# Kernel optimization log

Measured on AMD Instinct MI355X. Metric: run time of the kernel, lower is better.

Reference implementation:

```python
import jax, jax.numpy as jnp
import numpy as np

N = 32768; G = 64; PER = N // G; E = 262144; H = 128; HEADS = 4; DH = H // HEADS

def _leaky(x):
    return jnp.where(x > 0, x, 0.01 * x)

def _bn(x, w, b, eps=1e-5):
    mu = jnp.mean(x, 0)
    var = jnp.var(x, 0)  # biased, as torch BatchNorm1d uses for normalization
    return (x - mu) * jax.lax.rsqrt(var + eps) * w + b

def setup_inputs():
    key = jax.random.key(0)
    ks = jax.random.split(key, 20)
    s = 0.05
    g = jax.random.randint(ks[0], (E,), 0, G)
    src = g * PER + jax.random.randint(ks[1], (E,), 0, PER)
    dst = g * PER + jax.random.randint(ks[2], (E,), 0, PER)
    return {
        'node_fts': jax.random.normal(ks[3], (N, H)),
        'edge_attr': jax.random.normal(ks[4], (E, H)),
        'graph_fts': jax.random.normal(ks[5], (G, H)),
        'hidden': jax.random.normal(ks[6], (N, H)),
        'W_ee': jax.random.normal(ks[7], (H, H)) * s, 'b_ee': jnp.zeros((H,)),
        'M0': jax.random.normal(ks[8], (6 * H, H)) * s,
        'M1': jax.random.normal(ks[9], (H, H)) * s,
        'M2': jax.random.normal(ks[10], (H, H)) * s,
        'M3': jax.random.normal(ks[11], (H, H)) * s,
        'U1': jax.random.normal(ks[12], (2 * H, H)) * s,
        'U2': jax.random.normal(ks[13], (H, H)) * s,
        'Wqkv': jax.random.normal(ks[14], (H, 3 * H)) * s, 'bqkv': jnp.zeros((3 * H,)),
        'Wo': jax.random.normal(ks[15], (H, H)) * s, 'bo': jnp.zeros((H,)),
        'bn1_w': jnp.ones((H,)), 'bn1_b': jnp.zeros((H,)),
        'bn2_w': jnp.ones((H,)), 'bn2_b': jnp.zeros((H,)),
        'bn3_w': jnp.ones((H,)), 'bn3_b': jnp.zeros((H,)),
        'W1': jax.random.normal(ks[16], (H, 2 * H)) * s, 'b1': jnp.zeros((2 * H,)),
        'W2': jax.random.normal(ks[17], (2 * H, H)) * s, 'b2': jnp.zeros((H,)),
        'edge_index': jnp.stack([src, dst]),
        'batch': jnp.arange(N, dtype=jnp.int32) // PER,
    }

def _forward(node_fts, edge_attr, graph_fts, hidden, W_ee, b_ee, M0, M1, M2, M3,
             U1, U2, Wqkv, bqkv, Wo, bo, bn1_w, bn1_b, bn2_w, bn2_b,
             bn3_w, bn3_b, W1, b1, W2, b2, edge_index, batch):
    src, dst = edge_index[0], edge_index[1]
    ea = edge_attr @ W_ee + b_ee                            # GPS.edge_emb  [E,H]
    z = jnp.concatenate([node_fts, hidden], axis=-1)        # [N,2H]
    gfi = graph_fts[batch[dst]]                             # graph_fts_i   [E,H]
    # MPNN message: cat(x_i, x_j, edge_attr, graph_fts_i) -> 4-layer MLP, no bias
    m = jnp.concatenate([z[dst], z[src], ea, gfi], axis=-1) # [E,6H]
    m = m @ M0
    m = _leaky(m) @ M1
    m = _leaky(m) @ M2
    m = _leaky(m) @ M3                                      # [E,H]
    agg = jax.ops.segment_max(m, dst, num_segments=N)
    agg = jnp.where(jnp.isfinite(agg), agg, 0.0)            # PyG max-aggr: 0 for empty segments
    h_local = z @ U1 + agg @ U2                             # MPNN.update (use_gate=False)
    h1 = _bn(h_local + node_fts, bn1_w, bn1_b)              # GPSConv residual + norm1
    # global multihead attention over dense per-graph batches (all graphs exactly PER nodes)
    xd = node_fts.reshape(G, PER, H)
    q, k, v = jnp.split(xd @ Wqkv + bqkv, 3, axis=-1)
    q = q.reshape(G, PER, HEADS, DH).transpose(0, 2, 1, 3)
    k = k.reshape(G, PER, HEADS, DH).transpose(0, 2, 1, 3)
    v = v.reshape(G, PER, HEADS, DH).transpose(0, 2, 1, 3)
    att = jax.nn.softmax(jnp.einsum('ghqd,ghkd->ghqk', q, k) / float(np.sqrt(DH)), axis=-1)
    o = jnp.einsum('ghqk,ghkd->ghqd', att, v).transpose(0, 2, 1, 3).reshape(N, H)
    o = o @ Wo + bo
    h2 = _bn(o + node_fts, bn2_w, bn2_b)                    # residual + norm2
    out = h1 + h2
    out = out + (jax.nn.relu(out @ W1 + b1) @ W2 + b2)      # GPSConv MLP residual
    return _bn(out, bn3_w, bn3_b)                           # norm3

def reference(node_fts, edge_attr, graph_fts, hidden, W_ee, b_ee, M0, M1, M2, M3,
              U1, U2, Wqkv, bqkv, Wo, bo, bn1_w, bn1_b, bn2_w, bn2_b,
              bn3_w, bn3_b, W1, b1, W2, b2, edge_index, batch):
    return _forward(node_fts, edge_attr, graph_fts, hidden, W_ee, b_ee, M0, M1, M2, M3,
                    U1, U2, Wqkv, bqkv, Wo, bo, bn1_w, bn1_b, bn2_w, bn2_b,
                    bn3_w, bn3_b, W1, b1, W2, b2, edge_index, batch)
```

## Files before the change

### kernel.cpp

```cpp
#include <hip/hip_runtime.h>

typedef unsigned short u16;
typedef unsigned int u32;

#define NN 32768
#define EE 262144
#define HH 128
#define INV_N (1.0f / 32768.0f)
#define BN_EPS 1e-5f
#define ENC_NEGINF 0x007FFFFFu

typedef __attribute__((ext_vector_type(8))) __bf16 bf16x8;
typedef __attribute__((ext_vector_type(4))) float f32x4;

#define OFF_WEE 0
#define OFF_M0 16384
#define OFF_M1 114688
#define OFF_M2 131072
#define OFF_M3 147456
#define OFF_U 163840
#define OFF_QKV 212992
#define OFF_WO 262144
#define OFF_W1T 278528
#define OFF_W2T 311296
#define WT_ELEMS 344064

#define WS_AGG 0u
#define WS_OUTB 0u
#define WS_Y3 8388608u
#define WS_QKV 16777216u
#define WS_Y1 16777216u
#define WS_Y2 25165824u
#define WS_STATS 41943040u
#define WS_WT 41946112u

__device__ __forceinline__ float bf2f(u16 u) {
  union { u32 u; float f; } x; x.u = ((u32)u) << 16; return x.f;
}
__device__ __forceinline__ u16 f2bf(float f) {
  union { float f; u32 u; } x; x.f = f;
  return (u16)((x.u + 0x7FFFu + ((x.u >> 16) & 1u)) >> 16);
}
__device__ __forceinline__ u32 encf(float f) {
  union { float f; u32 u; } x; x.f = f;
  return (x.u & 0x80000000u) ? ~x.u : (x.u | 0x80000000u);
}
__device__ __forceinline__ float decf(u32 u) {
  union { u32 u; float f; } x;
  x.u = (u & 0x80000000u) ? (u ^ 0x80000000u) : ~u;
  return x.f;
}
__device__ __forceinline__ bf16x8 ld_frag(const u16* p) {
  return __builtin_bit_cast(bf16x8, *(const uint4*)p);
}
__device__ __forceinline__ uint4 pack8(const float* p) {
  u32 o0 = (u32)f2bf(p[0]) | ((u32)f2bf(p[1]) << 16);
  u32 o1 = (u32)f2bf(p[2]) | ((u32)f2bf(p[3]) << 16);
  u32 o2 = (u32)f2bf(p[4]) | ((u32)f2bf(p[5]) << 16);
  u32 o3 = (u32)f2bf(p[6]) | ((u32)f2bf(p[7]) << 16);
  return make_uint4(o0, o1, o2, o3);
}

template <int NCT>
__device__ __forceinline__ void mfma_step(const u16* As, int astride, int ka,
                                          const u16* Ws, int wstride, int kw,
                                          f32x4* acc, int lane, int wrow) {
  const int q = lane >> 4, cl = lane & 15;
  bf16x8 a = ld_frag(As + (wrow + cl) * astride + ka + q * 8);
#pragma unroll
  for (int ct = 0; ct < NCT; ++ct) {
    bf16x8 b = ld_frag(Ws + (ct * 16 + cl) * wstride + kw + q * 8);
    acc[ct] = __builtin_amdgcn_mfma_f32_16x16x32_bf16(a, b, acc[ct], 0, 0, 0);
  }
}

template <int NCT>
__device__ __forceinline__ void mfma_chunk128(const u16* A0, const u16* A1,
                                              const u16* Ws, int wstride,
                                              f32x4* acc, int lane, int wrow) {
  mfma_step<NCT>(A0, 72, 0, Ws, wstride, 0, acc, lane, wrow);
  mfma_step<NCT>(A0, 72, 32, Ws, wstride, 32, acc, lane, wrow);
  mfma_step<NCT>(A1, 72, 0, Ws, wstride, 64, acc, lane, wrow);
  mfma_step<NCT>(A1, 72, 32, Ws, wstride, 96, acc, lane, wrow);
}

__device__ __forceinline__ void stageA64f(u16* dst, const float* src, int rs, int tid) {
#pragma unroll
  for (int i = 0; i < 2; ++i) {
    int idx = tid + i * 256, r = idx >> 3, s = idx & 7;
    *(uint4*)(dst + r * 72 + s * 8) = pack8(src + (size_t)r * rs + s * 8);
  }
}
__device__ __forceinline__ void stageA64gf(u16* dst, const float* base,
                                           const int* rows, int co, int tid) {
#pragma unroll
  for (int i = 0; i < 2; ++i) {
    int idx = tid + i * 256, r = idx >> 3, s = idx & 7;
    *(uint4*)(dst + r * 72 + s * 8) = pack8(base + (size_t)rows[r] * HH + co + s * 8);
  }
}
__device__ __forceinline__ void stageA64(u16* dst, const u16* src, int rs, int tid) {
#pragma unroll
  for (int i = 0; i < 2; ++i) {
    int idx = tid + i * 256, r = idx >> 3, s = idx & 7;
    *(uint4*)(dst + r * 72 + s * 8) = *(const uint4*)(src + (size_t)r * rs + s * 8);
  }
}
__device__ __forceinline__ void stageA128(u16* dst, const u16* src, int tid) {
#pragma unroll
  for (int i = 0; i < 4; ++i) {
    int idx = tid + i * 256, r = idx >> 4, s = idx & 15;
    *(uint4*)(dst + r * 136 + s * 8) = *(const uint4*)(src + (size_t)r * HH + s * 8);
  }
}
template <int NR, int KW, int DS>
__device__ __forceinline__ void stageW(u16* dst, const u16* wt, int K, int koff, int tid) {
  constexpr int SEGS = KW / 8;
  constexpr int ITER = NR * SEGS / 256;
#pragma unroll
  for (int i = 0; i < ITER; ++i) {
    int idx = tid + i * 256;
    int c = idx / SEGS, s = idx % SEGS;
    *(uint4*)(dst + c * DS + s * 8) = *(const uint4*)(wt + (size_t)c * K + koff + s * 8);
  }
}
__device__ __forceinline__ void stage_agg(u16* dst, const u32* src, int tid) {
#pragma unroll
  for (int i = 0; i < 2; ++i) {
    int idx = tid + i * 256, r = idx >> 3, s = idx & 7;
    const u32* p = src + (size_t)r * HH + s * 8;
    u32 o[4];
#pragma unroll
    for (int j = 0; j < 4; ++j) {
      u32 u0 = p[2 * j], u1 = p[2 * j + 1];
      float f0 = (u0 == ENC_NEGINF) ? 0.f : decf(u0);
      float f1 = (u1 == ENC_NEGINF) ? 0.f : decf(u1);
      o[j] = (u32)f2bf(f0) | ((u32)f2bf(f1) << 16);
    }
    *(uint4*)(dst + r * 72 + s * 8) = make_uint4(o[0], o[1], o[2], o[3]);
  }
}


__global__ __launch_bounds__(256) void k_init(u32* __restrict__ agg,
                                              float* __restrict__ stats) {
  int gid = blockIdx.x * 256 + threadIdx.x;
  *(uint4*)(agg + (size_t)gid * 4) =
      make_uint4(ENC_NEGINF, ENC_NEGINF, ENC_NEGINF, ENC_NEGINF);
  if (gid < 768) stats[gid] = 0.f;
}

__global__ __launch_bounds__(256) void k_transpose(
    const float* w_ee, const float* m0, const float* m1, const float* m2,
    const float* m3, const float* u1, const float* u2, const float* wqkv,
    const float* wo, const float* w1, const float* w2, u16* __restrict__ wt) {
  const float* src; int K, C, ds, dk; size_t doff;
  switch (blockIdx.y) {
    case 0: src = w_ee; K = 128; C = 128; doff = OFF_WEE; ds = 128; dk = 0; break;
    case 1: src = m0; K = 768; C = 128; doff = OFF_M0; ds = 768; dk = 0; break;
    case 2: src = m1; K = 128; C = 128; doff = OFF_M1; ds = 128; dk = 0; break;
    case 3: src = m2; K = 128; C = 128; doff = OFF_M2; ds = 128; dk = 0; break;
    case 4: src = m3; K = 128; C = 128; doff = OFF_M3; ds = 128; dk = 0; break;
    case 5: src = u1; K = 256; C = 128; doff = OFF_U; ds = 384; dk = 0; break;
    case 6: src = u2; K = 128; C = 128; doff = OFF_U; ds = 384; dk = 256; break;
    case 7: src = wqkv; K = 128; C = 384; doff = OFF_QKV; ds = 128; dk = 0; break;
    case 8: src = wo; K = 128; C = 128; doff = OFF_WO; ds = 128; dk = 0; break;
    case 9: src = w1; K = 128; C = 256; doff = OFF_W1T; ds = 128; dk = 0; break;
    default: src = w2; K = 256; C = 128; doff = OFF_W2T; ds = 256; dk = 0; break;
  }
  int gid = blockIdx.x * 256 + threadIdx.x;
  if (gid < K * C) {
    int k = gid / C, c = gid - k * C;
    wt[doff + (size_t)c * ds + dk + k] = f2bf(src[gid]);
  }
}

__global__ __launch_bounds__(256) void k_edge(
    const float* __restrict__ node_fts, const float* __restrict__ hidden,
    const float* __restrict__ edge_attr, const float* __restrict__ graph_fts,
    const float* __restrict__ b_ee, const u16* __restrict__ wt,
    const int* __restrict__ ei, u32* __restrict__ agg) {
  __shared__ u16 sA0[64 * 72], sA1[64 * 72], sW[128 * 136];
  __shared__ int sSrc[64], sDst[64], sG[64];
  const int tid = threadIdx.x, lane = tid & 63, w = tid >> 6, wrow = w * 16;
  const int q = lane >> 4, cl = lane & 15;
  const int e0 = blockIdx.x * 64;
  if (tid < 64) {
    sSrc[tid] = ei[e0 + tid];
    int d = ei[EE + e0 + tid];
    sDst[tid] = d;
    sG[tid] = d >> 9;
  }
  stageA64f(sA0, edge_attr + (size_t)e0 * HH, HH, tid);
  stageA64f(sA1, edge_attr + (size_t)e0 * HH + 64, HH, tid);
  stageW<128, 128, 136>(sW, wt + OFF_WEE, 128, 0, tid);
  __syncthreads();
  const f32x4 fz = {0.f, 0.f, 0.f, 0.f};
  f32x4 acc[8];
#pragma unroll
  for (int i = 0; i < 8; ++i) acc[i] = fz;
  mfma_chunk128<8>(sA0, sA1, sW, 136, acc, lane, wrow);
#pragma unroll
  for (int ct = 0; ct < 8; ++ct) {
    float bias = b_ee[ct * 16 + cl];
#pragma unroll
    for (int r = 0; r < 4; ++r) {
      int row = wrow + q * 4 + r, col = ct * 16 + cl;
      u16* t = (col < 64) ? sA0 : sA1;
      t[row * 72 + (col & 63)] = f2bf(acc[ct][r] + bias);
    }
  }
  __syncthreads();
  stageW<128, 128, 136>(sW, wt + OFF_M0, 768, 512, tid);
  __syncthreads();
#pragma unroll
  for (int i = 0; i < 8; ++i) acc[i] = fz;
  mfma_chunk128<8>(sA0, sA1, sW, 136, acc, lane, wrow);
  const float* bs[5] = {node_fts, hidden, node_fts, hidden, graph_fts};
  const int* rw[5] = {sDst, sDst, sSrc, sSrc, sG};
  const int ko[5] = {0, 128, 256, 384, 640};
#pragma unroll
  for (int c = 0; c < 5; ++c) {
    __syncthreads();
    stageA64gf(sA0, bs[c], rw[c], 0, tid);
    stageA64gf(sA1, bs[c], rw[c], 64, tid);
    stageW<128, 128, 136>(sW, wt + OFF_M0, 768, ko[c], tid);
    __syncthreads();
    mfma_chunk128<8>(sA0, sA1, sW, 136, acc, lane, wrow);
  }
  const int lo[3] = {OFF_M1, OFF_M2, OFF_M3};
#pragma unroll
  for (int l = 0; l < 3; ++l) {
#pragma unroll
    for (int ct = 0; ct < 8; ++ct) {
#pragma unroll
      for (int r = 0; r < 4; ++r) {
        float v = acc[ct][r];
        v = v > 0.f ? v : 0.01f * v;
        int row = wrow + q * 4 + r, col = ct * 16 + cl;
        u16* t = (col < 64) ? sA0 : sA1;
        t[row * 72 + (col & 63)] = f2bf(v);
      }
    }
    __syncthreads();
    stageW<128, 128, 136>(sW, wt + lo[l], 128, 0, tid);
    __syncthreads();
#pragma unroll
    for (int i = 0; i < 8; ++i) acc[i] = fz;
    mfma_chunk128<8>(sA0, sA1, sW, 136, acc, lane, wrow);
  }
#pragma unroll
  for (int ct = 0; ct < 8; ++ct) {
#pragma unroll
    for (int r = 0; r < 4; ++r) {
      int e_l = wrow + q * 4 + r, f = ct * 16 + cl;
      atomicMax(&agg[(size_t)sDst[e_l] * HH + f], encf(acc[ct][r]));
    }
  }
}

__global__ __launch_bounds__(256) void k_y1(const float* __restrict__ node_fts,
                                            const float* __restrict__ hidden,
                                            const u32* __restrict__ agg,
                                            const u16* __restrict__ wt,
                                            u16* __restrict__ y1) {
  __shared__ u16 sA0[64 * 72], sA1[64 * 72], sW[128 * 136];
  const int tid = threadIdx.x, lane = tid & 63, w = tid >> 6, wrow = w * 16;
  const int q = lane >> 4, cl = lane & 15;
  const int nb = blockIdx.x * 64;
  const f32x4 fz = {0.f, 0.f, 0.f, 0.f};
  f32x4 acc[8];
#pragma unroll
  for (int i = 0; i < 8; ++i) acc[i] = fz;
  stageA64f(sA0, node_fts + (size_t)nb * HH, HH, tid);
  stageA64f(sA1, node_fts + (size_t)nb * HH + 64, HH, tid);
  stageW<128, 128, 136>(sW, wt + OFF_U, 384, 0, tid);
  __syncthreads();
  mfma_chunk128<8>(sA0, sA1, sW, 136, acc, lane, wrow);
  __syncthreads();
  stageA64f(sA0, hidden + (size_t)nb * HH, HH, tid);
  stageA64f(sA1, hidden + (size_t)nb * HH + 64, HH, tid);
  stageW<128, 128, 136>(sW, wt + OFF_U, 384, 128, tid);
  __syncthreads();
  mfma_chunk128<8>(sA0, sA1, sW, 136, acc, lane, wrow);
  __syncthreads();
  stage_agg(sA0, agg + (size_t)nb * HH, tid);
  stage_agg(sA1, agg + (size_t)nb * HH + 64, tid);
  stageW<128, 128, 136>(sW, wt + OFF_U, 384, 256, tid);
  __syncthreads();
  mfma_chunk128<8>(sA0, sA1, sW, 136, acc, lane, wrow);
#pragma unroll
  for (int ct = 0; ct < 8; ++ct) {
#pragma unroll
    for (int r = 0; r < 4; ++r) {
      int row = wrow + q * 4 + r, col = ct * 16 + cl;
      size_t gi = (size_t)(nb + row) * HH + col;
      y1[gi] = f2bf(acc[ct][r] + node_fts[gi]);
    }
  }
}

__global__ __launch_bounds__(256) void k_qkv(const float* __restrict__ node_fts,
                                             const u16* __restrict__ wt,
                                             const float* __restrict__ bqkv,
                                             u16* __restrict__ qkv) {
  __shared__ u16 sA0[64 * 72], sA1[64 * 72], sW[128 * 136];
  const int tid = threadIdx.x, lane = tid & 63, w = tid >> 6, wrow = w * 16;
  const int q = lane >> 4, cl = lane & 15;
  const int nb = blockIdx.x * 64;
  const f32x4 fz = {0.f, 0.f, 0.f, 0.f};
  stageA64f(sA0, node_fts + (size_t)nb * HH, HH, tid);
  stageA64f(sA1, node_fts + (size_t)nb * HH + 64, HH, tid);
#pragma unroll 1
  for (int cc = 0; cc < 3; ++cc) {
    if (cc) __syncthreads();
    stageW<128, 128, 136>(sW, wt + OFF_QKV + cc * 128 * 128, 128, 0, tid);
    __syncthreads();
    f32x4 acc[8];
#pragma unroll
    for (int i = 0; i < 8; ++i) acc[i] = fz;
    mfma_chunk128<8>(sA0, sA1, sW, 136, acc, lane, wrow);
#pragma unroll
    for (int ct = 0; ct < 8; ++ct) {
#pragma unroll
      for (int r = 0; r < 4; ++r) {
        int row = wrow + q * 4 + r, col = ct * 16 + cl;
        qkv[(size_t)(nb + row) * 384 + cc * 128 + col] =
            f2bf(acc[ct][r] + bqkv[cc * 128 + col]);
      }
    }
  }
}

#define SPW (32 * 136)
__global__ __launch_bounds__(256) void k_attn(const u16* __restrict__ qkv,
                                              u16* __restrict__ oatt) {
  __shared__ u16 sK[128 * 40];
  __shared__ u16 sVt[32 * 136];
  __shared__ u16 sP[4 * SPW];
  const int tid = threadIdx.x, lane = tid & 63, w = tid >> 6;
  const int q = lane >> 4, cl = lane & 15;
  const int bx = blockIdx.x;
  const int g = bx >> 4, h = (bx >> 2) & 3, qt = bx & 3;
  const u16* base = qkv + (size_t)g * 512 * 384;
  const int q0 = qt * 128 + w * 32;
  const float scale = 0.17677669529663687f;
  bf16x8 qa[2];
#pragma unroll
  for (int t = 0; t < 2; ++t)
    qa[t] = ld_frag(base + (size_t)(q0 + t * 16 + cl) * 384 + h * 32 + q * 8);
  const f32x4 fz = {0.f, 0.f, 0.f, 0.f};
  f32x4 accO[2][2];
  float m_[2][4], l_[2][4];
#pragma unroll
  for (int t = 0; t < 2; ++t) {
    accO[t][0] = fz;
    accO[t][1] = fz;
#pragma unroll
    for (int r = 0; r < 4; ++r) {
      m_[t][r] = -3.4e38f;
      l_[t][r] = 0.f;
    }
  }
  u16* myP = sP + w * SPW;
#pragma unroll 1
  for (int kt = 0; kt < 4; ++kt) {
    __syncthreads();
#pragma unroll
    for (int i = 0; i < 2; ++i) {
      int ii = tid + i * 256, r = ii >> 2, s = ii & 3;
      *(uint4*)(sK + r * 40 + s * 8) =
          *(const uint4*)(base + (size_t)(kt * 128 + r) * 384 + 128 + h * 32 + s * 8);
    }
#pragma unroll
    for (int i = 0; i < 2; ++i) {
      int ii = tid + i * 256, r = ii >> 2, s = ii & 3;
      uint4 v = *(const uint4*)(base + (size_t)(kt * 128 + r) * 384 + 256 + h * 32 + s * 8);
      u32 a[4] = {v.x, v.y, v.z, v.w};
#pragma unroll
      for (int j = 0; j < 4; ++j) {
        sVt[(s * 8 + 2 * j) * 136 + r] = (u16)a[j];
        sVt[(s * 8 + 2 * j + 1) * 136 + r] = (u16)(a[j] >> 16);
      }
    }
    __syncthreads();
    f32x4 accS[2][8];
#pragma unroll
    for (int ct = 0; ct < 8; ++ct) {
      bf16x8 b = ld_frag(sK + (ct * 16 + cl) * 40 + q * 8);
      accS[0][ct] = __builtin_amdgcn_mfma_f32_16x16x32_bf16(qa[0], b, fz, 0, 0, 0);
      accS[1][ct] = __builtin_amdgcn_mfma_f32_16x16x32_bf16(qa[1], b, fz, 0, 0, 0);
    }
#pragma unroll
    for (int t = 0; t < 2; ++t) {
#pragma unroll
      for (int r = 0; r < 4; ++r) {
        float mx = accS[t][0][r];
#pragma unroll
        for (int ct = 1; ct < 8; ++ct) mx = fmaxf(mx, accS[t][ct][r]);
        mx = fmaxf(mx, __shfl_xor(mx, 1));
        mx = fmaxf(mx, __shfl_xor(mx, 2));
        mx = fmaxf(mx, __shfl_xor(mx, 4));
        mx = fmaxf(mx, __shfl_xor(mx, 8));
        float mn = fmaxf(m_[t][r], mx * scale);
        float f = __expf(m_[t][r] - mn);
        m_[t][r] = mn;
        float rs = 0.f;
#pragma unroll
        for (int ct = 0; ct < 8; ++ct) {
          float p = __expf(accS[t][ct][r] * scale - mn);
          accS[t][ct][r] = p;
          rs += p;
        }
        rs += __shfl_xor(rs, 1);
        rs += __shfl_xor(rs, 2);
        rs += __shfl_xor(rs, 4);
        rs += __shfl_xor(rs, 8);
        l_[t][r] = l_[t][r] * f + rs;
        accO[t][0][r] *= f;
        accO[t][1][r] *= f;
      }
    }
#pragma unroll
    for (int t = 0; t < 2; ++t)
#pragma unroll
      for (int ct = 0; ct < 8; ++ct)
#pragma unroll
        for (int r = 0; r < 4; ++r)
          myP[(t * 16 + q * 4 + r) * 136 + ct * 16 + cl] = f2bf(accS[t][ct][r]);
#pragma unroll
    for (int kk = 0; kk < 4; ++kk) {
      bf16x8 pa0 = ld_frag(myP + (size_t)cl * 136 + kk * 32 + q * 8);
      bf16x8 pa1 = ld_frag(myP + (size_t)(16 + cl) * 136 + kk * 32 + q * 8);
#pragma unroll
      for (int c = 0; c < 2; ++c) {
        bf16x8 b = ld_frag(sVt + (c * 16 + cl) * 136 + kk * 32 + q * 8);
        accO[0][c] = __builtin_amdgcn_mfma_f32_16x16x32_bf16(pa0, b, accO[0][c], 0, 0, 0);
        accO[1][c] = __builtin_amdgcn_mfma_f32_16x16x32_bf16(pa1, b, accO[1][c], 0, 0, 0);
      }
    }
  }
#pragma unroll
  for (int t = 0; t < 2; ++t)
#pragma unroll
    for (int r = 0; r < 4; ++r) {
      float il = 1.f / l_[t][r];
      int row = g * 512 + q0 + t * 16 + q * 4 + r;
#pragma unroll
      for (int c = 0; c < 2; ++c)
        oatt[(size_t)row * HH + h * 32 + c * 16 + cl] = f2bf(accO[t][c][r] * il);
    }
}

__global__ __launch_bounds__(256) void k_y2(const u16* __restrict__ oatt,
                                            const float* __restrict__ node_fts,
                                            const u16* __restrict__ wt,
                                            const float* __restrict__ bo,
                                            u16* __restrict__ y2) {
  __shared__ u16 sA0[64 * 72], sA1[64 * 72], sW[128 * 136];
  const int tid = threadIdx.x, lane = tid & 63, w = tid >> 6, wrow = w * 16;
  const int q = lane >> 4, cl = lane & 15;
  const int nb = blockIdx.x * 64;
  const f32x4 fz = {0.f, 0.f, 0.f, 0.f};
  f32x4 acc[8];
#pragma unroll
  for (int i = 0; i < 8; ++i) acc[i] = fz;
  stageA64(sA0, oatt + (size_t)nb * HH, HH, tid);
  stageA64(sA1, oatt + (size_t)nb * HH + 64, HH, tid);
  stageW<128, 128, 136>(sW, wt + OFF_WO, 128, 0, tid);
  __syncthreads();
  mfma_chunk128<8>(sA0, sA1, sW, 136, acc, lane, wrow);
#pragma unroll
  for (int ct = 0; ct < 8; ++ct) {
#pragma unroll
    for (int r = 0; r < 4; ++r) {
      int row = wrow + q * 4 + r, col = ct * 16 + cl;
      size_t gi = (size_t)(nb + row) * HH + col;
      y2[gi] = f2bf(acc[ct][r] + bo[col] + node_fts[gi]);
    }
  }
}

__global__ __launch_bounds__(256) void k_stats(const u16* __restrict__ y,
                                               float* __restrict__ sum,
                                               float* __restrict__ sq) {
  const int tid = threadIdx.x, f = tid & 127, rh = tid >> 7;
  const int rb = blockIdx.x * 64;
  float s = 0.f, s2 = 0.f;
  for (int i = 0; i < 32; ++i) {
    float v = bf2f(y[(size_t)(rb + rh + 2 * i) * HH + f]);
    s += v;
    s2 += v * v;
  }
  __shared__ float bs[256], bq[256];
  bs[tid] = s;
  bq[tid] = s2;
  __syncthreads();
  if (tid < 128) {
    atomicAdd(&sum[f], bs[tid] + bs[tid + 128]);
    atomicAdd(&sq[f], bq[tid] + bq[tid + 128]);
  }
}

__global__ __launch_bounds__(256) void k_combine(
    const u16* __restrict__ y1, const u16* __restrict__ y2,
    const float* __restrict__ stats, const float* __restrict__ w1,
    const float* __restrict__ b1, const float* __restrict__ w2,
    const float* __restrict__ b2, u16* __restrict__ outb) {
  int i4 = blockIdx.x * 256 + threadIdx.x;
  uint2 a2 = *(const uint2*)(y1 + (size_t)i4 * 4);
  uint2 b2v = *(const uint2*)(y2 + (size_t)i4 * 4);
  u16 av[4] = {(u16)a2.x, (u16)(a2.x >> 16), (u16)a2.y, (u16)(a2.y >> 16)};
  u16 bv[4] = {(u16)b2v.x, (u16)(b2v.x >> 16), (u16)b2v.y, (u16)(b2v.y >> 16)};
  int f0 = (i4 & 31) * 4;
  u16 o[4];
#pragma unroll
  for (int j = 0; j < 4; ++j) {
    int f = f0 + j;
    float mu1 = stats[f] * INV_N;
    float v1 = stats[128 + f] * INV_N - mu1 * mu1;
    float r1 = rsqrtf(v1 + BN_EPS);
    float mu2 = stats[256 + f] * INV_N;
    float v2 = stats[384 + f] * INV_N - mu2 * mu2;
    float r2 = rsqrtf(v2 + BN_EPS);
    float val = (bf2f(av[j]) - mu1) * r1 * w1[f] + b1[f] +
                (bf2f(bv[j]) - mu2) * r2 * w2[f] + b2[f];
    o[j] = f2bf(val);
  }
  u32 lo2 = (u32)o[0] | ((u32)o[1] << 16);
  u32 hi2 = (u32)o[2] | ((u32)o[3] << 16);
  *(uint2*)(outb + (size_t)i4 * 4) = make_uint2(lo2, hi2);
}

__global__ __launch_bounds__(256) void k_mlp(const u16* __restrict__ outb,
                                             const u16* __restrict__ wt,
                                             const float* __restrict__ b1,
                                             const float* __restrict__ b2,
                                             u16* __restrict__ y3) {
  __shared__ u16 sA[64 * 136];
  __shared__ u16 sW[128 * 136];
  __shared__ u16 sI[64 * 72];
  const int tid = threadIdx.x, lane = tid & 63, w = tid >> 6, wrow = w * 16;
  const int q = lane >> 4, cl = lane & 15;
  const int nb = blockIdx.x * 64;
  const f32x4 fz = {0.f, 0.f, 0.f, 0.f};
  stageA128(sA, outb + (size_t)nb * HH, tid);
  f32x4 acc3[8];
#pragma unroll
  for (int i = 0; i < 8; ++i) acc3[i] = fz;
#pragma unroll 1
  for (int cc = 0; cc < 4; ++cc) {
    __syncthreads();
    stageW<64, 128, 136>(sW, wt + OFF_W1T + cc * 64 * 128, 128, 0, tid);
    __syncthreads();
    f32x4 a1[4];
#pragma unroll
    for (int i = 0; i < 4; ++i) a1[i] = fz;
    mfma_step<4>(sA, 136, 0, sW, 136, 0, a1, lane, wrow);
    mfma_step<4>(sA, 136, 32, sW, 136, 32, a1, lane, wrow);
    mfma_step<4>(sA, 136, 64, sW, 136, 64, a1, lane, wrow);
    mfma_step<4>(sA, 136, 96, sW, 136, 96, a1, lane, wrow);
#pragma unroll
    for (int ct = 0; ct < 4; ++ct) {
      float bias = b1[cc * 64 + ct * 16 + cl];
#pragma unroll
      for (int r = 0; r < 4; ++r) {
        float v = fmaxf(a1[ct][r] + bias, 0.f);
        sI[(wrow + q * 4 + r) * 72 + ct * 16 + cl] = f2bf(v);
      }
    }
    __syncthreads();
    stageW<128, 64, 72>(sW, wt + OFF_W2T, 256, cc * 64, tid);
    __syncthreads();
    mfma_step<8>(sI, 72, 0, sW, 72, 0, acc3, lane, wrow);
    mfma_step<8>(sI, 72, 32, sW, 72, 32, acc3, lane, wrow);
  }
#pragma unroll
  for (int ct = 0; ct < 8; ++ct) {
#pragma unroll
    for (int r = 0; r < 4; ++r) {
      int row = wrow + q * 4 + r, col = ct * 16 + cl;
      size_t gi = (size_t)(nb + row) * HH + col;
      y3[gi] = f2bf(acc3[ct][r] + b2[col] + bf2f(outb[gi]));
    }
  }
}

__global__ __launch_bounds__(256) void k_final(const u16* __restrict__ y3,
                                               const float* __restrict__ sum3,
                                               const float* __restrict__ sq3,
                                               const float* __restrict__ w3,
                                               const float* __restrict__ b3,
                                               float* __restrict__ out) {
  int i4 = blockIdx.x * 256 + threadIdx.x;
  uint2 a2 = *(const uint2*)(y3 + (size_t)i4 * 4);
  u16 av[4] = {(u16)a2.x, (u16)(a2.x >> 16), (u16)a2.y, (u16)(a2.y >> 16)};
  int f0 = (i4 & 31) * 4;
  float o[4];
#pragma unroll
  for (int j = 0; j < 4; ++j) {
    int f = f0 + j;
    float mu = sum3[f] * INV_N;
    float var = sq3[f] * INV_N - mu * mu;
    float r = rsqrtf(var + BN_EPS);
    o[j] = (bf2f(av[j]) - mu) * r * w3[f] + b3[f];
  }
  *(float4*)(out + (size_t)i4 * 4) = make_float4(o[0], o[1], o[2], o[3]);
}

extern "C" void kernel_launch(void* const* d_in, const int* in_sizes, int n_in,
                              void* d_out, int out_size, void* d_ws, size_t ws_size,
                              hipStream_t stream) {
  (void)in_sizes; (void)n_in; (void)out_size; (void)ws_size;
  const float* node_fts = (const float*)d_in[0];
  const float* edge_attr = (const float*)d_in[1];
  const float* graph_fts = (const float*)d_in[2];
  const float* hidden = (const float*)d_in[3];
  const float* W_ee = (const float*)d_in[4];
  const float* b_ee = (const float*)d_in[5];
  const float* M0 = (const float*)d_in[6];
  const float* M1 = (const float*)d_in[7];
  const float* M2 = (const float*)d_in[8];
  const float* M3 = (const float*)d_in[9];
  const float* U1 = (const float*)d_in[10];
  const float* U2 = (const float*)d_in[11];
  const float* Wqkv = (const float*)d_in[12];
  const float* bqkv = (const float*)d_in[13];
  const float* Wo = (const float*)d_in[14];
  const float* bo = (const float*)d_in[15];
  const float* bn1w = (const float*)d_in[16];
  const float* bn1b = (const float*)d_in[17];
  const float* bn2w = (const float*)d_in[18];
  const float* bn2b = (const float*)d_in[19];
  const float* bn3w = (const float*)d_in[20];
  const float* bn3b = (const float*)d_in[21];
  const float* W1 = (const float*)d_in[22];
  const float* b1 = (const float*)d_in[23];
  const float* W2 = (const float*)d_in[24];
  const float* b2 = (const float*)d_in[25];
  const int* ei = (const int*)d_in[26];

  char* ws = (char*)d_ws;
  u32* agg = (u32*)(ws + WS_AGG);
  u16* outb = (u16*)(ws + WS_OUTB);
  u16* y3 = (u16*)(ws + WS_Y3);
  u16* qkv = (u16*)(ws + WS_QKV);
  u16* y1 = (u16*)(ws + WS_Y1);
  u16* y2 = (u16*)(ws + WS_Y2);
  float* stats = (float*)(ws + WS_STATS);
  u16* wt = (u16*)(ws + WS_WT);
  u16* oatt = (u16*)d_out;
  float* out = (float*)d_out;

  k_init<<<4096, 256, 0, stream>>>(agg, stats);
  k_transpose<<<dim3(384, 11), 256, 0, stream>>>(W_ee, M0, M1, M2, M3, U1, U2,
                                                 Wqkv, Wo, W1, W2, wt);
  k_edge<<<4096, 256, 0, stream>>>(node_fts, hidden, edge_attr, graph_fts, b_ee,
                                   wt, ei, agg);
  k_qkv<<<512, 256, 0, stream>>>(node_fts, wt, bqkv, qkv);
  k_attn<<<1024, 256, 0, stream>>>(qkv, oatt);
  k_y1<<<512, 256, 0, stream>>>(node_fts, hidden, agg, wt, y1);
  k_y2<<<512, 256, 0, stream>>>(oatt, node_fts, wt, bo, y2);
  k_stats<<<512, 256, 0, stream>>>(y1, stats + 0, stats + 128);
  k_stats<<<512, 256, 0, stream>>>(y2, stats + 256, stats + 384);
  k_combine<<<4096, 256, 0, stream>>>(y1, y2, stats, bn1w, bn1b, bn2w, bn2b, outb);
  k_mlp<<<512, 256, 0, stream>>>(outb, wt, b1, b2, y3);
  k_stats<<<512, 256, 0, stream>>>(y3, stats + 512, stats + 640);
  k_final<<<4096, 256, 0, stream>>>(y3, stats + 512, stats + 640, bn3w, bn3b, out);
}
```

Baseline: 607.4 us.

## Restructure edge kernel: direct-register A fragments, prefetched weight tiles, packed bf16 conversion

The edge MLP kernel now loads each A fragment directly from global fp32 rows into registers and converts it there, instead of staging gathered rows through shared memory. Weight tiles for the next chunk are prefetched into registers while the current chunk's MFMAs run, and the layer loop is no longer unrolled. Occupancy is raised with launch bounds (256,3), and fp32-to-bf16 packing uses the hardware cvt_pk builtin when available. The aim is to cut shared-memory traffic and global-load latency stalls, at the cost of more registers and uncoalesced per-lane gathers.

```diff
diff --git a/kernel.cpp b/kernel.cpp
--- a/kernel.cpp
+++ b/kernel.cpp
@@ -11,6 +11,7 @@
 #define ENC_NEGINF 0x007FFFFFu
 
 typedef __attribute__((ext_vector_type(8))) __bf16 bf16x8;
+typedef __attribute__((ext_vector_type(2))) __bf16 bf16x2;
 typedef __attribute__((ext_vector_type(4))) float f32x4;
 
 #define OFF_WEE 0
@@ -41,6 +42,14 @@
   union { float f; u32 u; } x; x.f = f;
   return (u16)((x.u + 0x7FFFu + ((x.u >> 16) & 1u)) >> 16);
 }
+__device__ __forceinline__ u32 pk2bf(float a, float b) {
+#if __has_builtin(__builtin_amdgcn_cvt_pk_bf16_f32)
+  bf16x2 r = __builtin_amdgcn_cvt_pk_bf16_f32(a, b);
+  return __builtin_bit_cast(u32, r);
+#else
+  return (u32)f2bf(a) | ((u32)f2bf(b) << 16);
+#endif
+}
 __device__ __forceinline__ u32 encf(float f) {
   union { float f; u32 u; } x; x.f = f;
   return (x.u & 0x80000000u) ? ~x.u : (x.u | 0x80000000u);
@@ -54,11 +63,13 @@
   return __builtin_bit_cast(bf16x8, *(const uint4*)p);
 }
 __device__ __forceinline__ uint4 pack8(const float* p) {
-  u32 o0 = (u32)f2bf(p[0]) | ((u32)f2bf(p[1]) << 16);
-  u32 o1 = (u32)f2bf(p[2]) | ((u32)f2bf(p[3]) << 16);
-  u32 o2 = (u32)f2bf(p[4]) | ((u32)f2bf(p[5]) << 16);
-  u32 o3 = (u32)f2bf(p[6]) | ((u32)f2bf(p[7]) << 16);
-  return make_uint4(o0, o1, o2, o3);
+  float4 x = *(const float4*)p;
+  float4 y = *(const float4*)(p + 4);
+  return make_uint4(pk2bf(x.x, x.y), pk2bf(x.z, x.w), pk2bf(y.x, y.y),
+                    pk2bf(y.z, y.w));
+}
+__device__ __forceinline__ bf16x8 cvt8(const float* p) {
+  return __builtin_bit_cast(bf16x8, pack8(p));
 }
 
 template <int NCT>
@@ -91,14 +102,6 @@
     *(uint4*)(dst + r * 72 + s * 8) = pack8(src + (size_t)r * rs + s * 8);
   }
 }
-__device__ __forceinline__ void stageA64gf(u16* dst, const float* base,
-                                           const int* rows, int co, int tid) {
-#pragma unroll
-  for (int i = 0; i < 2; ++i) {
-    int idx = tid + i * 256, r = idx >> 3, s = idx & 7;
-    *(uint4*)(dst + r * 72 + s * 8) = pack8(base + (size_t)rows[r] * HH + co + s * 8);
-  }
-}
 __device__ __forceinline__ void stageA64(u16* dst, const u16* src, int rs, int tid) {
 #pragma unroll
   for (int i = 0; i < 2; ++i) {
@@ -135,7 +138,7 @@
       u32 u0 = p[2 * j], u1 = p[2 * j + 1];
       float f0 = (u0 == ENC_NEGINF) ? 0.f : decf(u0);
       float f1 = (u1 == ENC_NEGINF) ? 0.f : decf(u1);
-      o[j] = (u32)f2bf(f0) | ((u32)f2bf(f1) << 16);
+      o[j] = pk2bf(f0, f1);
     }
     *(uint4*)(dst + r * 72 + s * 8) = make_uint4(o[0], o[1], o[2], o[3]);
   }
@@ -175,87 +178,135 @@
   }
 }
 
-__global__ __launch_bounds__(256) void k_edge(
+#define TS 136
+
+__device__ __forceinline__ void prefB(uint4* r, const u16* bp, int K, int koff,
+                                      int bc0, int bs) {
+#pragma unroll
+  for (int i = 0; i < 8; ++i)
+    r[i] = *(const uint4*)(bp + (size_t)(bc0 + i * 16) * K + koff + bs * 8);
+}
+__device__ __forceinline__ void writeB(u16* sB, const uint4* r, int bc0, int bs) {
+#pragma unroll
+  for (int i = 0; i < 8; ++i)
+    *(uint4*)(sB + (bc0 + i * 16) * TS + bs * 8) = r[i];
+}
+__device__ __forceinline__ void chunkF(f32x4* acc, const float* row,
+                                       const u16* sB, int cl, int q) {
+#pragma unroll
+  for (int ks = 0; ks < 4; ++ks) {
+    bf16x8 a = cvt8(row + ks * 32 + q * 8);
+#pragma unroll
+    for (int ct = 0; ct < 8; ++ct) {
+      bf16x8 b = ld_frag(sB + (ct * 16 + cl) * TS + ks * 32 + q * 8);
+      acc[ct] = __builtin_amdgcn_mfma_f32_16x16x32_bf16(a, b, acc[ct], 0, 0, 0);
+    }
+  }
+}
+__device__ __forceinline__ void chunkL(f32x4* acc, const u16* myT,
+                                       const u16* sB, int cl, int q) {
+#pragma unroll
+  for (int ks = 0; ks < 4; ++ks) {
+    bf16x8 a = ld_frag(myT + cl * TS + ks * 32 + q * 8);
+#pragma unroll
+    for (int ct = 0; ct < 8; ++ct) {
+      bf16x8 b = ld_frag(sB + (ct * 16 + cl) * TS + ks * 32 + q * 8);
+      acc[ct] = __builtin_amdgcn_mfma_f32_16x16x32_bf16(a, b, acc[ct], 0, 0, 0);
+    }
+  }
+}
+
+__global__ __launch_bounds__(256, 3) void k_edge(
     const float* __restrict__ node_fts, const float* __restrict__ hidden,
     const float* __restrict__ edge_attr, const float* __restrict__ graph_fts,
     const float* __restrict__ b_ee, const u16* __restrict__ wt,
     const int* __restrict__ ei, u32* __restrict__ agg) {
-  __shared__ u16 sA0[64 * 72], sA1[64 * 72], sW[128 * 136];
-  __shared__ int sSrc[64], sDst[64], sG[64];
-  const int tid = threadIdx.x, lane = tid & 63, w = tid >> 6, wrow = w * 16;
+  __shared__ u16 sB[128 * TS];
+  __shared__ u16 sT[4 * 16 * TS];
+  const int tid = threadIdx.x, lane = tid & 63, w = tid >> 6;
   const int q = lane >> 4, cl = lane & 15;
   const int e0 = blockIdx.x * 64;
-  if (tid < 64) {
-    sSrc[tid] = ei[e0 + tid];
-    int d = ei[EE + e0 + tid];
-    sDst[tid] = d;
-    sG[tid] = d >> 9;
-  }
-  stageA64f(sA0, edge_attr + (size_t)e0 * HH, HH, tid);
-  stageA64f(sA1, edge_attr + (size_t)e0 * HH + 64, HH, tid);
-  stageW<128, 128, 136>(sW, wt + OFF_WEE, 128, 0, tid);
-  __syncthreads();
+  const int erow = e0 + w * 16 + cl;
+  const int src = ei[erow];
+  const int dst = ei[EE + erow];
+  const int grow = dst >> 9;
+  const int bs = tid & 15, bc0 = tid >> 4;
+  u16* myT = sT + w * 16 * TS;
   const f32x4 fz = {0.f, 0.f, 0.f, 0.f};
   f32x4 acc[8];
+  uint4 bpre[8];
+
+  prefB(bpre, wt + OFF_WEE, 128, 0, bc0, bs);
+  writeB(sB, bpre, bc0, bs);
+  __syncthreads();
+  prefB(bpre, wt + OFF_M0, 768, 0, bc0, bs);
 #pragma unroll
   for (int i = 0; i < 8; ++i) acc[i] = fz;
-  mfma_chunk128<8>(sA0, sA1, sW, 136, acc, lane, wrow);
+  chunkF(acc, edge_attr + (size_t)erow * HH, sB, cl, q);
 #pragma unroll
   for (int ct = 0; ct < 8; ++ct) {
     float bias = b_ee[ct * 16 + cl];
 #pragma unroll
-    for (int r = 0; r < 4; ++r) {
-      int row = wrow + q * 4 + r, col = ct * 16 + cl;
-      u16* t = (col < 64) ? sA0 : sA1;
-      t[row * 72 + (col & 63)] = f2bf(acc[ct][r] + bias);
-    }
-  }
-  __syncthreads();
-  stageW<128, 128, 136>(sW, wt + OFF_M0, 768, 512, tid);
-  __syncthreads();
+    for (int r = 0; r < 4; ++r)
+      myT[(q * 4 + r) * TS + ct * 16 + cl] = f2bf(acc[ct][r] + bias);
+  }
 #pragma unroll
   for (int i = 0; i < 8; ++i) acc[i] = fz;
-  mfma_chunk128<8>(sA0, sA1, sW, 136, acc, lane, wrow);
-  const float* bs[5] = {node_fts, hidden, node_fts, hidden, graph_fts};
-  const int* rw[5] = {sDst, sDst, sSrc, sSrc, sG};
-  const int ko[5] = {0, 128, 256, 384, 640};
-#pragma unroll
-  for (int c = 0; c < 5; ++c) {
-    __syncthreads();
-    stageA64gf(sA0, bs[c], rw[c], 0, tid);
-    stageA64gf(sA1, bs[c], rw[c], 64, tid);
-    stageW<128, 128, 136>(sW, wt + OFF_M0, 768, ko[c], tid);
-    __syncthreads();
-    mfma_chunk128<8>(sA0, sA1, sW, 136, acc, lane, wrow);
-  }
+  __syncthreads();
+  writeB(sB, bpre, bc0, bs);
+  __syncthreads();
+  prefB(bpre, wt + OFF_M0, 768, 128, bc0, bs);
+  chunkF(acc, node_fts + (size_t)dst * HH, sB, cl, q);
+  __syncthreads();
+  writeB(sB, bpre, bc0, bs);
+  __syncthreads();
+  prefB(bpre, wt + OFF_M0, 768, 256, bc0, bs);
+  chunkF(acc, hidden + (size_t)dst * HH, sB, cl, q);
+  __syncthreads();
+  writeB(sB, bpre, bc0, bs);
+  __syncthreads();
+  prefB(bpre, wt + OFF_M0, 768, 384, bc0, bs);
+  chunkF(acc, node_fts + (size_t)src * HH, sB, cl, q);
+  __syncthreads();
+  writeB(sB, bpre, bc0, bs);
+  __syncthreads();
+  prefB(bpre, wt + OFF_M0, 768, 512, bc0, bs);
+  chunkF(acc, hidden + (size_t)src * HH, sB, cl, q);
+  __syncthreads();
+  writeB(sB, bpre, bc0, bs);
+  __syncthreads();
+  prefB(bpre, wt + OFF_M0, 768, 640, bc0, bs);
+  chunkL(acc, myT, sB, cl, q);
+  __syncthreads();
+  writeB(sB, bpre, bc0, bs);
+  __syncthreads();
+  prefB(bpre, wt + OFF_M1, 128, 0, bc0, bs);
+  chunkF(acc, graph_fts + (size_t)grow * HH, sB, cl, q);
   const int lo[3] = {OFF_M1, OFF_M2, OFF_M3};
-#pragma unroll
+#pragma unroll 1
   for (int l = 0; l < 3; ++l) {
 #pragma unroll
-    for (int ct = 0; ct < 8; ++ct) {
+    for (int ct = 0; ct < 8; ++ct)
 #pragma unroll
       for (int r = 0; r < 4; ++r) {
         float v = acc[ct][r];
         v = v > 0.f ? v : 0.01f * v;
-        int row = wrow + q * 4 + r, col = ct * 16 + cl;
-        u16* t = (col < 64) ? sA0 : sA1;
-        t[row * 72 + (col & 63)] = f2bf(v);
+        myT[(q * 4 + r) * TS + ct * 16 + cl] = f2bf(v);
       }
-    }
-    __syncthreads();
-    stageW<128, 128, 136>(sW, wt + lo[l], 128, 0, tid);
-    __syncthreads();
+    __syncthreads();
+    writeB(sB, bpre, bc0, bs);
+    __syncthreads();
+    if (l < 2) prefB(bpre, wt + lo[l + 1], 128, 0, bc0, bs);
 #pragma unroll
     for (int i = 0; i < 8; ++i) acc[i] = fz;
-    mfma_chunk128<8>(sA0, sA1, sW, 136, acc, lane, wrow);
-  }
-#pragma unroll
-  for (int ct = 0; ct < 8; ++ct) {
-#pragma unroll
-    for (int r = 0; r < 4; ++r) {
-      int e_l = wrow + q * 4 + r, f = ct * 16 + cl;
-      atomicMax(&agg[(size_t)sDst[e_l] * HH + f], encf(acc[ct][r]));
-    }
+    chunkL(acc, myT, sB, cl, q);
+  }
+#pragma unroll
+  for (int r = 0; r < 4; ++r) {
+    int d_r = __shfl(dst, q * 4 + r);
+#pragma unroll
+    for (int ct = 0; ct < 8; ++ct)
+      atomicMax(&agg[(size_t)d_r * HH + ct * 16 + cl], encf(acc[ct][r]));
   }
 }
 
```

After: 926.9 us. +52.6%, slower.
